# Kernel optimization log

Hardware: AMD Instinct MI355X
Metric: run time of the kernel (lower is better)

The kernel has to match this reference:

```python
import jax, jax.numpy as jnp
import numpy as np

N_NODES = 100000
N_EDGES = 1600000
N_GRAPHS = 512
DIM = 64


def gcn_conv(x, W, b, src, dst, n):
    # PyG GCNConv: h = x @ W; add self-loops; symmetric norm D^-1/2 (A+I) D^-1/2; aggregate; + bias
    h = x @ W  # [N, H]
    loop = jnp.arange(n, dtype=src.dtype)
    s = jnp.concatenate([src, loop])
    d = jnp.concatenate([dst, loop])
    deg = jax.ops.segment_sum(jnp.ones_like(d, dtype=h.dtype), d, num_segments=n)  # in-degree incl self-loop
    dinv = jnp.where(deg > 0, jax.lax.rsqrt(deg), 0.0)
    norm = dinv[s] * dinv[d]  # [E+N]
    msg = h[s] * norm[:, None]  # gather + scale
    out = jax.ops.segment_sum(msg, d, num_segments=n)  # scatter-add
    return out + b


def global_mean_pool(x, batch, num_graphs):
    sums = jax.ops.segment_sum(x, batch, num_segments=num_graphs)
    cnts = jax.ops.segment_sum(jnp.ones((x.shape[0],), x.dtype), batch, num_segments=num_graphs)
    return sums / jnp.maximum(cnts, 1.0)[:, None]


def setup_inputs() -> dict:
    key = jax.random.key(0)
    ks = jax.random.split(key, 12)
    scale = 1.0 / np.sqrt(DIM)
    x = jax.random.normal(ks[0], (N_NODES, DIM), jnp.float32)
    edge_index = jax.random.randint(ks[1], (2, N_EDGES), 0, N_NODES, dtype=jnp.int64)
    batch = jnp.sort(jax.random.randint(ks[2], (N_NODES,), 0, N_GRAPHS, dtype=jnp.int64))
    W1 = jax.random.normal(ks[3], (DIM, DIM), jnp.float32) * scale
    b1 = jnp.zeros((DIM,), jnp.float32)
    W2 = jax.random.normal(ks[4], (DIM, DIM), jnp.float32) * scale
    b2 = jnp.zeros((DIM,), jnp.float32)
    W3 = jax.random.normal(ks[5], (DIM, DIM), jnp.float32) * scale
    b3 = jnp.zeros((DIM,), jnp.float32)
    W4 = jax.random.normal(ks[6], (DIM, 1), jnp.float32) * scale
    b4 = jnp.zeros((1,), jnp.float32)
    return {"x": x, "edge_index": edge_index, "batch": batch,
            "W1": W1, "b1": b1, "W2": W2, "b2": b2,
            "W3": W3, "b3": b3, "W4": W4, "b4": b4}


def reference(x, edge_index, batch, W1, b1, W2, b2, W3, b3, W4, b4):
    src, dst = edge_index[0], edge_index[1]
    h = gcn_conv(x, W1, b1, src, dst, N_NODES)
    h = jax.nn.relu(h)
    h = gcn_conv(h, W2, b2, src, dst, N_NODES)
    g = global_mean_pool(h, batch, N_GRAPHS)  # [G, H]
    g = jax.nn.relu(g @ W3 + b3)
    pred = (g @ W4 + b4).reshape(-1)  # [G]
    return pred
```

## Files before the change

### kernel.cpp

```cpp
#include <hip/hip_runtime.h>
#include <hip/hip_fp16.h>
#include <math.h>


#define NBLK 3125

__global__ __launch_bounds__(256) void k_init(float* gsum, int* blockCnt,
                                              int gsz, int nblk) {
  int i = blockIdx.x * 256 + threadIdx.x;
  if (i < gsz) gsum[i] = 0.f;
  if (i < nblk + 64) blockCnt[i] = 0;
}

__global__ __launch_bounds__(256) void k_histB(const int* __restrict__ dst,
                                               int* __restrict__ blockCnt,
                                               int e, int nblk) {
  __shared__ int h[3200];
  int t = threadIdx.x;
  for (int i = t; i < 3200; i += 256) h[i] = 0;
  __syncthreads();
  int base = blockIdx.x * 8192;
#pragma unroll
  for (int k = 0; k < 32; ++k) {
    int i = base + k * 256 + t;
    if (i < e) atomicAdd(&h[dst[i] >> 5], 1);
  }
  __syncthreads();
  for (int i = t; i < nblk; i += 256) {
    int v = h[i];
    if (v) atomicAdd(&blockCnt[i], v);
  }
}

__global__ __launch_bounds__(256) void k_scan(const int* __restrict__ blockCnt,
                                              int* __restrict__ blockBase,
                                              int* __restrict__ blockCursor,
                                              int* __restrict__ bucketCursor,
                                              int nblk, int nbuck) {
  __shared__ int wsum[4];
  int t = threadIdx.x;
  int w = t >> 6, lane = t & 63;
  int ch = (nblk + 255) >> 8;
  int lo = t * ch;
  int hi = lo + ch;
  if (hi > nblk) hi = nblk;
  int s = 0;
  for (int i = lo; i < hi; ++i) s += blockCnt[i];
  int inc = s;
  for (int off = 1; off < 64; off <<= 1) {
    int u = __shfl_up(inc, off);
    if (lane >= off) inc += u;
  }
  if (lane == 63) wsum[w] = inc;
  __syncthreads();
  int wpre = 0;
  for (int i = 0; i < w; ++i) wpre += wsum[i];
  int run = wpre + inc - s;
  for (int i = lo; i < hi; ++i) {
    int v = blockCnt[i];
    blockBase[i] = run;
    blockCursor[i] = run;
    if ((i & 63) == 0 && (i >> 6) < nbuck) bucketCursor[i >> 6] = run;
    run += v;
  }
  if (t == 0) blockBase[nblk] = wsum[0] + wsum[1] + wsum[2] + wsum[3];
}

__global__ __launch_bounds__(256) void k_p1(const int* __restrict__ src,
                                            const int* __restrict__ dst,
                                            int* __restrict__ bucketCursor,
                                            int* __restrict__ tmp, int e) {
  __shared__ int hist[64];
  __shared__ int gbase[64];
  int t = threadIdx.x;
  int base = blockIdx.x * 2048;
  if (t < 64) hist[t] = 0;
  __syncthreads();
  int ent[8], rk[8], bk[8];
#pragma unroll
  for (int k = 0; k < 8; ++k) {
    int i = base + k * 256 + t;
    bool v = i < e;
    int s = v ? src[i] : 0;
    int d = v ? dst[i] : 0;
    bk[k] = d >> 11;
    ent[k] = (((d >> 5) & 63) << 22) | (s << 5) | (d & 31);
    rk[k] = v ? atomicAdd(&hist[bk[k]], 1) : -1;
  }
  __syncthreads();
  if (t < 64 && hist[t] > 0) gbase[t] = atomicAdd(&bucketCursor[t], hist[t]);
  __syncthreads();
#pragma unroll
  for (int k = 0; k < 8; ++k)
    if (rk[k] >= 0) tmp[gbase[bk[k]] + rk[k]] = ent[k];
}

__global__ __launch_bounds__(256) void k_p2(const int* __restrict__ blockBase,
                                            const int* __restrict__ tmp,
                                            int* __restrict__ blockCursor,
                                            int* __restrict__ csr, int nblk) {
  __shared__ int hist[64];
  __shared__ int gbase[64];
  int b = blockIdx.x >> 3;
  int sl = blockIdx.x & 7;
  int hiIdx = (b + 1) << 6;
  if (hiIdx > nblk) hiIdx = nblk;
  int lo_b = blockBase[b << 6];
  int hi_b = blockBase[hiIdx];
  int len = hi_b - lo_b;
  int lo = lo_b + (int)(((long long)len * sl) >> 3);
  int hi = lo_b + (int)(((long long)len * (sl + 1)) >> 3);
  int t = threadIdx.x;
  for (int rbase = lo; rbase < hi; rbase += 2048) {
    if (t < 64) hist[t] = 0;
    __syncthreads();
    int ent[8], rk[8], bin[8];
#pragma unroll
    for (int k = 0; k < 8; ++k) {
      int i = rbase + k * 256 + t;
      bool v = i < hi;
      int en = v ? tmp[i] : 0;
      ent[k] = en;
      bin[k] = en >> 22;
      rk[k] = v ? atomicAdd(&hist[bin[k]], 1) : -1;
    }
    __syncthreads();
    if (t < 64 && hist[t] > 0)
      gbase[t] = atomicAdd(&blockCursor[(b << 6) + t], hist[t]);
    __syncthreads();
#pragma unroll
    for (int k = 0; k < 8; ++k)
      if (rk[k] >= 0) csr[gbase[bin[k]] + rk[k]] = ent[k] & 0x3FFFFF;
    __syncthreads();
  }
}

__global__ __launch_bounds__(256) void k_bsort(const int* __restrict__ blockBase,
                                               int* __restrict__ csr,
                                               float* __restrict__ dinv,
                                               int* __restrict__ segLo,
                                               int* __restrict__ segHi,
                                               const float* __restrict__ x,
                                               __half* __restrict__ P16, int n) {
  __shared__ int in_sh[1024];
  __shared__ int out_sh[1024];
  __shared__ int hist[128];
  __shared__ int hscan[128];
  __shared__ int deg[32];
  __shared__ float sdinv[32];
  int blk = blockIdx.x;
  int nodeBase = blk << 5;
  if (nodeBase >= n) return;
  int p0 = blockBase[blk];
  int p1 = blockBase[blk + 1];
  int seg = p1 - p0;
  int t = threadIdx.x;
  if (t < 32) deg[t] = 0;
  if (t == 0) {
    segLo[2 * blk] = p0;
    segHi[2 * blk] = p1;
    segLo[2 * blk + 1] = p0;
    segHi[2 * blk + 1] = p1;
  }
  __syncthreads();
  for (int i = t; i < seg; i += 256) atomicAdd(&deg[csr[p0 + i] & 31], 1);
  __syncthreads();
  if (t < 32 && nodeBase + t < n) {
    float dv = 1.0f / sqrtf((float)(deg[t] + 1));
    dinv[nodeBase + t] = dv;
    sdinv[t] = dv;
  }
  __syncthreads();
  for (int i = t; i < 1024; i += 256) {
    int row = i >> 5, h2 = (i & 31) << 1;
    int node = nodeBase + row;
    if (node < n) {
      float2 v = *(const float2*)&x[(size_t)node * 64 + h2];
      float sdv = sdinv[row];
      *(__half2*)&P16[(size_t)node * 64 + h2] =
          __floats2half2_rn(v.x * sdv, v.y * sdv);
    }
  }
  if (seg <= 0 || seg > 1024) return;
  if (t < 128) hist[t] = 0;
  __syncthreads();
  for (int i = t; i < seg; i += 256) {
    int v = csr[p0 + i];
    in_sh[i] = v;
    atomicAdd(&hist[((v & 16) << 2) | ((v >> 16) & 63)], 1);
  }
  __syncthreads();
  if (t < 64) {
    int h0 = hist[2 * t], h1 = hist[2 * t + 1];
    int s = h0 + h1;
    int inc = s;
    for (int off = 1; off < 64; off <<= 1) {
      int u = __shfl_up(inc, off);
      if (t >= off) inc += u;
    }
    hscan[2 * t] = inc - s;
    hscan[2 * t + 1] = inc - s + h0;
  }
  __syncthreads();
  int cntLow = hscan[64];
  __syncthreads();
  for (int i = t; i < seg; i += 256) {
    int v = in_sh[i];
    int pos = atomicAdd(&hscan[((v & 16) << 2) | ((v >> 16) & 63)], 1);
    out_sh[pos] = v;
  }
  __syncthreads();
  for (int i = t; i < seg; i += 256) csr[p0 + i] = out_sh[i];
  if (t == 0) {
    segHi[2 * blk] = p0 + cntLow;
    segLo[2 * blk + 1] = p0 + cntLow;
  }
}

__global__ __launch_bounds__(256) void k_gemm64brs(const float* __restrict__ X,
                                                   const float* __restrict__ W,
                                                   const float* __restrict__ bias,
                                                   const float* __restrict__ dinv,
                                                   __half* __restrict__ Y16, int n) {
  __shared__ float Xs[64 * 65];
  __shared__ float Ws[64 * 64];
  int t = threadIdx.x;
  int r0 = blockIdx.x << 6;
  for (int i = t * 4; i < 4096; i += 1024)
    *(float4*)&Ws[i] = *(const float4*)&W[i];
  for (int s = t; s < 1024; s += 256) {
    int r = s >> 4, c4 = (s & 15) << 2;
    float4 v = make_float4(0.f, 0.f, 0.f, 0.f);
    if (r0 + r < n) v = *(const float4*)&X[(size_t)(r0 + r) * 64 + c4];
    Xs[r * 65 + c4 + 0] = v.x;
    Xs[r * 65 + c4 + 1] = v.y;
    Xs[r * 65 + c4 + 2] = v.z;
    Xs[r * 65 + c4 + 3] = v.w;
  }
  __syncthreads();
  int c4 = (t & 15) << 2;
  int rb = (t >> 4) << 2;
  float4 a0 = {0, 0, 0, 0}, a1 = {0, 0, 0, 0}, a2 = {0, 0, 0, 0}, a3 = {0, 0, 0, 0};
  for (int k = 0; k < 64; ++k) {
    float4 w = *(const float4*)&Ws[k * 64 + c4];
    float x0 = Xs[(rb + 0) * 65 + k];
    float x1 = Xs[(rb + 1) * 65 + k];
    float x2 = Xs[(rb + 2) * 65 + k];
    float x3 = Xs[(rb + 3) * 65 + k];
    a0.x += x0 * w.x; a0.y += x0 * w.y; a0.z += x0 * w.z; a0.w += x0 * w.w;
    a1.x += x1 * w.x; a1.y += x1 * w.y; a1.z += x1 * w.z; a1.w += x1 * w.w;
    a2.x += x2 * w.x; a2.y += x2 * w.y; a2.z += x2 * w.z; a2.w += x2 * w.w;
    a3.x += x3 * w.x; a3.y += x3 * w.y; a3.z += x3 * w.z; a3.w += x3 * w.w;
  }
  float4 bb = *(const float4*)&bias[c4];
  int r = r0 + rb;
  union { __half2 h[2]; uint2 u; } pk;
  if (r + 0 < n) {
    float s0 = dinv[r + 0];
    pk.h[0] = __floats2half2_rn(fmaxf(a0.x + bb.x, 0.f) * s0,
                                fmaxf(a0.y + bb.y, 0.f) * s0);
    pk.h[1] = __floats2half2_rn(fmaxf(a0.z + bb.z, 0.f) * s0,
                                fmaxf(a0.w + bb.w, 0.f) * s0);
    *(uint2*)&Y16[(size_t)(r + 0) * 64 + c4] = pk.u;
  }
  if (r + 1 < n) {
    float s1 = dinv[r + 1];
    pk.h[0] = __floats2half2_rn(fmaxf(a1.x + bb.x, 0.f) * s1,
                                fmaxf(a1.y + bb.y, 0.f) * s1);
    pk.h[1] = __floats2half2_rn(fmaxf(a1.z + bb.z, 0.f) * s1,
                                fmaxf(a1.w + bb.w, 0.f) * s1);
    *(uint2*)&Y16[(size_t)(r + 1) * 64 + c4] = pk.u;
  }
  if (r + 2 < n) {
    float s2 = dinv[r + 2];
    pk.h[0] = __floats2half2_rn(fmaxf(a2.x + bb.x, 0.f) * s2,
                                fmaxf(a2.y + bb.y, 0.f) * s2);
    pk.h[1] = __floats2half2_rn(fmaxf(a2.z + bb.z, 0.f) * s2,
                                fmaxf(a2.w + bb.w, 0.f) * s2);
    *(uint2*)&Y16[(size_t)(r + 2) * 64 + c4] = pk.u;
  }
  if (r + 3 < n) {
    float s3 = dinv[r + 3];
    pk.h[0] = __floats2half2_rn(fmaxf(a3.x + bb.x, 0.f) * s3,
                                fmaxf(a3.y + bb.y, 0.f) * s3);
    pk.h[1] = __floats2half2_rn(fmaxf(a3.z + bb.z, 0.f) * s3,
                                fmaxf(a3.w + bb.w, 0.f) * s3);
    *(uint2*)&Y16[(size_t)(r + 3) * 64 + c4] = pk.u;
  }
}

template <int POOL>
__global__ __launch_bounds__(128) void k_agg(
    const __half* __restrict__ Xh, const int* __restrict__ csr,
    const int* __restrict__ segLo, const int* __restrict__ segHi,
    const float* __restrict__ dinv, const int* __restrict__ batch,
    float* __restrict__ outv, float* __restrict__ gsum, int n, int ntask) {
  __shared__ float accs[2][16 * 64];
  int t = threadIdx.x;
  int w = t >> 6, lane = t & 63;
  int task = blockIdx.x * 2 + w;
  if (task >= ntask) return;
  int nodeBase = task << 4;
  int par = task & 1;
  float* a = accs[w];
#pragma unroll 4
  for (int d = 0; d < 16; ++d) a[d * 64 + lane] = 0.f;
  int p0 = segLo[task];
  int p1 = segHi[task];
  int c = p1 - p0;
  if (c > 0) {
    int sub = lane & 31;
    int qlast = p1 - 1;
    int qq = p0 + sub;
    int pk = csr[qq < qlast ? qq : qlast];
    for (int rb = 0; rb < c; rb += 32) {
      int pk_next = 0;
      bool more = (rb + 32) < c;
      if (more) {
        int qn = p0 + rb + 32 + sub;
        pk_next = csr[qn < qlast ? qn : qlast];
      }
      int rem = c - rb;
      int ee[32];
#pragma unroll
      for (int k = 0; k < 32; ++k) ee[k] = __builtin_amdgcn_readlane(pk, k);
      __half tv[32];
#pragma unroll
      for (int k = 0; k < 32; ++k)
        tv[k] = Xh[(size_t)(ee[k] >> 5) * 64 + lane];
#pragma unroll
      for (int k = 0; k < 32; ++k)
        if (k < rem && (((ee[k] >> 4) & 1) == par))
          a[(ee[k] & 15) * 64 + lane] += __half2float(tv[k]);
      pk = pk_next;
    }
  }
  for (int d = 0; d < 16; ++d) {
    int node = nodeBase + d;
    if (node >= n) break;
    float dn = dinv[node];
    float xv = __half2float(Xh[(size_t)node * 64 + lane]);
    float v = (a[d * 64 + lane] + xv) * dn;
    if (POOL) {
      int g = batch[node];
      atomicAdd(&gsum[(size_t)g * 64 + lane], v);
    } else {
      outv[(size_t)node * 64 + lane] = v;
    }
  }
}

__global__ __launch_bounds__(256) void k_head(
    const float* __restrict__ gsum, const int* __restrict__ batch,
    const float* __restrict__ W2, const float* __restrict__ b2,
    const float* __restrict__ W3, const float* __restrict__ b3,
    const float* __restrict__ W4, const float* __restrict__ b4,
    float* __restrict__ out, int ng, int n) {
  int wid = (blockIdx.x * 256 + threadIdx.x) >> 6;
  int lane = threadIdx.x & 63;
  if (wid >= ng) return;
  int lo = 0, hi = n;
  while (lo < hi) {
    int mid = (lo + hi) >> 1;
    if (batch[mid] < wid) lo = mid + 1; else hi = mid;
  }
  int lb = lo;
  hi = n;
  while (lo < hi) {
    int mid = (lo + hi) >> 1;
    if (batch[mid] <= wid) lo = mid + 1; else hi = mid;
  }
  float cden = fmaxf((float)(lo - lb), 1.0f);
  float m = gsum[(size_t)wid * 64 + lane] / cden;
  float g2 = b2[lane];
  for (int k = 0; k < 64; ++k) {
    float mk = __shfl(m, k);
    g2 += mk * W2[k * 64 + lane];
  }
  float g3 = b3[lane];
  for (int k = 0; k < 64; ++k) {
    float gk = __shfl(g2, k);
    g3 += gk * W3[k * 64 + lane];
  }
  g3 = fmaxf(g3, 0.f);
  float r = g3 * W4[lane];
  for (int off = 32; off; off >>= 1) r += __shfl_down(r, off);
  if (lane == 0) out[wid] = r + b4[0];
}

extern "C" void kernel_launch(void* const* d_in, const int* in_sizes, int n_in,
                              void* d_out, int out_size, void* d_ws, size_t ws_size,
                              hipStream_t stream) {
  const float* x = (const float*)d_in[0];
  const int* edge = (const int*)d_in[1];
  const int* batch = (const int*)d_in[2];
  const float* W1 = (const float*)d_in[3];
  const float* b1 = (const float*)d_in[4];
  const float* W2 = (const float*)d_in[5];
  const float* b2 = (const float*)d_in[6];
  const float* W3 = (const float*)d_in[7];
  const float* b3 = (const float*)d_in[8];
  const float* W4 = (const float*)d_in[9];
  const float* b4 = (const float*)d_in[10];
  float* out = (float*)d_out;

  const int n = in_sizes[0] / 64;
  const int e = in_sizes[1] / 2;
  const int ng = out_size;
  const int* src = edge;
  const int* dst = edge + e;

  char* ws = (char*)d_ws;
  size_t off = 0;
  auto alloc = [&](size_t bytes) -> void* {
    void* p = ws + off;
    off = (off + bytes + 255) & ~(size_t)255;
    return p;
  };
  __half* A16 = (__half*)alloc((size_t)n * 64 * 2);
  float* B = (float*)alloc((size_t)n * 64 * 4);
  float* dinv = (float*)alloc((size_t)n * 4);
  int* blockCnt = (int*)alloc(3264 * 4);
  int* blockBase = (int*)alloc(3264 * 4);
  int* blockCursor = (int*)alloc(3264 * 4);
  int* bucketCursor = (int*)alloc(64 * 4);
  int* segLo = (int*)alloc(6400 * 4);
  int* segHi = (int*)alloc(6400 * 4);
  int* csr = (int*)alloc((size_t)e * 4);
  float* gsum = (float*)alloc((size_t)ng * 64 * 4);
  int* tmp = (int*)B;

  const int nblk = (n + 31) / 32;
  const int nbuck = (nblk + 63) / 64;
  const int ntask = 2 * nblk;
  const int nagg = (ntask + 1) / 2;
  const int gsz = ng * 64;

  int zmax = gsz > nblk + 64 ? gsz : nblk + 64;
  k_init<<<(zmax + 255) / 256, 256, 0, stream>>>(gsum, blockCnt, gsz, nblk);
  k_histB<<<(e + 8191) / 8192, 256, 0, stream>>>(dst, blockCnt, e, nblk);
  k_scan<<<1, 256, 0, stream>>>(blockCnt, blockBase, blockCursor, bucketCursor,
                                nblk, nbuck);
  k_p1<<<(e + 2047) / 2048, 256, 0, stream>>>(src, dst, bucketCursor, tmp, e);
  k_p2<<<nbuck * 8, 256, 0, stream>>>(blockBase, tmp, blockCursor, csr, nblk);
  k_bsort<<<nblk, 256, 0, stream>>>(blockBase, csr, dinv, segLo, segHi, x, A16, n);

  k_agg<0><<<nagg, 128, 0, stream>>>(A16, csr, segLo, segHi, dinv, batch, B,
                                     gsum, n, ntask);
  k_gemm64brs<<<(n + 63) / 64, 256, 0, stream>>>(B, W1, b1, dinv, A16, n);
  k_agg<1><<<nagg, 128, 0, stream>>>(A16, csr, segLo, segHi, dinv, batch, B,
                                     gsum, n, ntask);
  k_head<<<((size_t)ng * 64 + 255) / 256, 256, 0, stream>>>(
      gsum, batch, W2, b2, W3, b3, W4, b4, out, ng, n);
}
```

Before: 305.5 us.

## Interleave fp16 feature layout so aggregation gathers two edges per wave instruction

```diff
diff --git a/kernel.cpp b/kernel.cpp
--- a/kernel.cpp
+++ b/kernel.cpp
@@ -19,9 +19,9 @@
   int t = threadIdx.x;
   for (int i = t; i < 3200; i += 256) h[i] = 0;
   __syncthreads();
-  int base = blockIdx.x * 8192;
-#pragma unroll
-  for (int k = 0; k < 32; ++k) {
+  int base = blockIdx.x * 16384;
+#pragma unroll
+  for (int k = 0; k < 64; ++k) {
     int i = base + k * 256 + t;
     if (i < e) atomicAdd(&h[dst[i] >> 5], 1);
   }
@@ -171,14 +171,17 @@
     sdinv[t] = dv;
   }
   __syncthreads();
-  for (int i = t; i < 1024; i += 256) {
-    int row = i >> 5, h2 = (i & 31) << 1;
+  for (int i = t; i < 512; i += 256) {
+    int row = i >> 4, q2 = (i & 15) << 1;
     int node = nodeBase + row;
     if (node < n) {
-      float2 v = *(const float2*)&x[(size_t)node * 64 + h2];
-      float sdv = sdinv[row];
-      *(__half2*)&P16[(size_t)node * 64 + h2] =
-          __floats2half2_rn(v.x * sdv, v.y * sdv);
+      float2 lo = *(const float2*)&x[(size_t)node * 64 + q2];
+      float2 hi = *(const float2*)&x[(size_t)node * 64 + q2 + 32];
+      float s = sdinv[row];
+      union { __half2 h[2]; uint2 u; } pk;
+      pk.h[0] = __floats2half2_rn(lo.x * s, hi.x * s);
+      pk.h[1] = __floats2half2_rn(lo.y * s, hi.y * s);
+      *(uint2*)&P16[(size_t)node * 64 + (q2 << 1)] = pk.u;
     }
   }
   if (seg <= 0 || seg > 1024) return;
@@ -238,54 +241,56 @@
     Xs[r * 65 + c4 + 3] = v.w;
   }
   __syncthreads();
-  int c4 = (t & 15) << 2;
+  int q = t & 15;
   int rb = (t >> 4) << 2;
   float4 a0 = {0, 0, 0, 0}, a1 = {0, 0, 0, 0}, a2 = {0, 0, 0, 0}, a3 = {0, 0, 0, 0};
   for (int k = 0; k < 64; ++k) {
-    float4 w = *(const float4*)&Ws[k * 64 + c4];
+    float2 wlo = *(const float2*)&Ws[k * 64 + 2 * q];
+    float2 whi = *(const float2*)&Ws[k * 64 + 2 * q + 32];
     float x0 = Xs[(rb + 0) * 65 + k];
     float x1 = Xs[(rb + 1) * 65 + k];
     float x2 = Xs[(rb + 2) * 65 + k];
     float x3 = Xs[(rb + 3) * 65 + k];
-    a0.x += x0 * w.x; a0.y += x0 * w.y; a0.z += x0 * w.z; a0.w += x0 * w.w;
-    a1.x += x1 * w.x; a1.y += x1 * w.y; a1.z += x1 * w.z; a1.w += x1 * w.w;
-    a2.x += x2 * w.x; a2.y += x2 * w.y; a2.z += x2 * w.z; a2.w += x2 * w.w;
-    a3.x += x3 * w.x; a3.y += x3 * w.y; a3.z += x3 * w.z; a3.w += x3 * w.w;
-  }
-  float4 bb = *(const float4*)&bias[c4];
+    a0.x += x0 * wlo.x; a0.y += x0 * wlo.y; a0.z += x0 * whi.x; a0.w += x0 * whi.y;
+    a1.x += x1 * wlo.x; a1.y += x1 * wlo.y; a1.z += x1 * whi.x; a1.w += x1 * whi.y;
+    a2.x += x2 * wlo.x; a2.y += x2 * wlo.y; a2.z += x2 * whi.x; a2.w += x2 * whi.y;
+    a3.x += x3 * wlo.x; a3.y += x3 * wlo.y; a3.z += x3 * whi.x; a3.w += x3 * whi.y;
+  }
+  float2 bblo = *(const float2*)&bias[2 * q];
+  float2 bbhi = *(const float2*)&bias[2 * q + 32];
   int r = r0 + rb;
   union { __half2 h[2]; uint2 u; } pk;
   if (r + 0 < n) {
     float s0 = dinv[r + 0];
-    pk.h[0] = __floats2half2_rn(fmaxf(a0.x + bb.x, 0.f) * s0,
-                                fmaxf(a0.y + bb.y, 0.f) * s0);
-    pk.h[1] = __floats2half2_rn(fmaxf(a0.z + bb.z, 0.f) * s0,
-                                fmaxf(a0.w + bb.w, 0.f) * s0);
-    *(uint2*)&Y16[(size_t)(r + 0) * 64 + c4] = pk.u;
+    pk.h[0] = __floats2half2_rn(fmaxf(a0.x + bblo.x, 0.f) * s0,
+                                fmaxf(a0.z + bbhi.x, 0.f) * s0);
+    pk.h[1] = __floats2half2_rn(fmaxf(a0.y + bblo.y, 0.f) * s0,
+                                fmaxf(a0.w + bbhi.y, 0.f) * s0);
+    *(uint2*)&Y16[(size_t)(r + 0) * 64 + 4 * q] = pk.u;
   }
   if (r + 1 < n) {
     float s1 = dinv[r + 1];
-    pk.h[0] = __floats2half2_rn(fmaxf(a1.x + bb.x, 0.f) * s1,
-                                fmaxf(a1.y + bb.y, 0.f) * s1);
-    pk.h[1] = __floats2half2_rn(fmaxf(a1.z + bb.z, 0.f) * s1,
-                                fmaxf(a1.w + bb.w, 0.f) * s1);
-    *(uint2*)&Y16[(size_t)(r + 1) * 64 + c4] = pk.u;
+    pk.h[0] = __floats2half2_rn(fmaxf(a1.x + bblo.x, 0.f) * s1,
+                                fmaxf(a1.z + bbhi.x, 0.f) * s1);
+    pk.h[1] = __floats2half2_rn(fmaxf(a1.y + bblo.y, 0.f) * s1,
+                                fmaxf(a1.w + bbhi.y, 0.f) * s1);
+    *(uint2*)&Y16[(size_t)(r + 1) * 64 + 4 * q] = pk.u;
   }
   if (r + 2 < n) {
     float s2 = dinv[r + 2];
-    pk.h[0] = __floats2half2_rn(fmaxf(a2.x + bb.x, 0.f) * s2,
-                                fmaxf(a2.y + bb.y, 0.f) * s2);
-    pk.h[1] = __floats2half2_rn(fmaxf(a2.z + bb.z, 0.f) * s2,
-                                fmaxf(a2.w + bb.w, 0.f) * s2);
-    *(uint2*)&Y16[(size_t)(r + 2) * 64 + c4] = pk.u;
+    pk.h[0] = __floats2half2_rn(fmaxf(a2.x + bblo.x, 0.f) * s2,
+                                fmaxf(a2.z + bbhi.x, 0.f) * s2);
+    pk.h[1] = __floats2half2_rn(fmaxf(a2.y + bblo.y, 0.f) * s2,
+                                fmaxf(a2.w + bbhi.y, 0.f) * s2);
+    *(uint2*)&Y16[(size_t)(r + 2) * 64 + 4 * q] = pk.u;
   }
   if (r + 3 < n) {
     float s3 = dinv[r + 3];
-    pk.h[0] = __floats2half2_rn(fmaxf(a3.x + bb.x, 0.f) * s3,
-                                fmaxf(a3.y + bb.y, 0.f) * s3);
-    pk.h[1] = __floats2half2_rn(fmaxf(a3.z + bb.z, 0.f) * s3,
-                                fmaxf(a3.w + bb.w, 0.f) * s3);
-    *(uint2*)&Y16[(size_t)(r + 3) * 64 + c4] = pk.u;
+    pk.h[0] = __floats2half2_rn(fmaxf(a3.x + bblo.x, 0.f) * s3,
+                                fmaxf(a3.z + bbhi.x, 0.f) * s3);
+    pk.h[1] = __floats2half2_rn(fmaxf(a3.y + bblo.y, 0.f) * s3,
+                                fmaxf(a3.w + bbhi.y, 0.f) * s3);
+    *(uint2*)&Y16[(size_t)(r + 3) * 64 + 4 * q] = pk.u;
   }
 }
 
@@ -310,6 +315,7 @@
   int c = p1 - p0;
   if (c > 0) {
     int sub = lane & 31;
+    int h = lane >> 5;
     int qlast = p1 - 1;
     int qq = p0 + sub;
     int pk = csr[qq < qlast ? qq : qlast];
@@ -321,17 +327,41 @@
         pk_next = csr[qn < qlast ? qn : qlast];
       }
       int rem = c - rb;
-      int ee[32];
-#pragma unroll
-      for (int k = 0; k < 32; ++k) ee[k] = __builtin_amdgcn_readlane(pk, k);
-      __half tv[32];
-#pragma unroll
-      for (int k = 0; k < 32; ++k)
-        tv[k] = Xh[(size_t)(ee[k] >> 5) * 64 + lane];
-#pragma unroll
-      for (int k = 0; k < 32; ++k)
-        if (k < rem && (((ee[k] >> 4) & 1) == par))
-          a[(ee[k] & 15) * 64 + lane] += __half2float(tv[k]);
+      int e0[16], e1[16];
+#pragma unroll
+      for (int k = 0; k < 16; ++k) {
+        e0[k] = __builtin_amdgcn_readlane(pk, 2 * k);
+        e1[k] = __builtin_amdgcn_readlane(pk, 2 * k + 1);
+      }
+      unsigned tu[16];
+#pragma unroll
+      for (int k = 0; k < 16; ++k) {
+        int esel = h ? e1[k] : e0[k];
+        tu[k] = *(const unsigned*)&Xh[(size_t)(esel >> 5) * 64 + (sub << 1)];
+      }
+#pragma unroll
+      for (int k = 0; k < 16; ++k) {
+        bool ok0 = (2 * k < rem) && (((e0[k] >> 4) & 1) == par);
+        bool ok1 = (2 * k + 1 < rem) && (((e1[k] >> 4) & 1) == par);
+        int d0 = e0[k] & 15, d1 = e1[k] & 15;
+        __half2 hv = *(__half2*)&tu[k];
+        float2 f = __half22float2(hv);
+        if (ok0 && ok1 && d0 == d1) {
+          float ox = __shfl(f.x, sub + 32);
+          float oy = __shfl(f.y, sub + 32);
+          if (h == 0) {
+            a[d0 * 64 + sub] += f.x + ox;
+            a[d0 * 64 + sub + 32] += f.y + oy;
+          }
+        } else {
+          bool ok = h ? ok1 : ok0;
+          int d = h ? d1 : d0;
+          if (ok) {
+            a[d * 64 + sub] += f.x;
+            a[d * 64 + sub + 32] += f.y;
+          }
+        }
+      }
       pk = pk_next;
     }
   }
@@ -339,7 +369,8 @@
     int node = nodeBase + d;
     if (node >= n) break;
     float dn = dinv[node];
-    float xv = __half2float(Xh[(size_t)node * 64 + lane]);
+    int pidx = ((lane & 31) << 1) | (lane >> 5);
+    float xv = __half2float(Xh[(size_t)node * 64 + pidx]);
     float v = (a[d * 64 + lane] + xv) * dn;
     if (POOL) {
       int g = batch[node];
@@ -438,7 +469,7 @@
 
   int zmax = gsz > nblk + 64 ? gsz : nblk + 64;
   k_init<<<(zmax + 255) / 256, 256, 0, stream>>>(gsum, blockCnt, gsz, nblk);
-  k_histB<<<(e + 8191) / 8192, 256, 0, stream>>>(dst, blockCnt, e, nblk);
+  k_histB<<<(e + 16383) / 16384, 256, 0, stream>>>(dst, blockCnt, e, nblk);
   k_scan<<<1, 256, 0, stream>>>(blockCnt, blockBase, blockCursor, bucketCursor,
                                 nblk, nbuck);
   k_p1<<<(e + 2047) / 2048, 256, 0, stream>>>(src, dst, bucketCursor, tmp, e);
```

After: 323.3 us. +5.8%, slower.

## Fuse destination histogram into bucket partition pass with fixed-capacity buckets

Applied to the files above, without the earlier changes.

```diff
diff --git a/kernel.cpp b/kernel.cpp
--- a/kernel.cpp
+++ b/kernel.cpp
@@ -4,39 +4,21 @@
 
 
 #define NBLK 3125
+#define BCAP 40960
 
 __global__ __launch_bounds__(256) void k_init(float* gsum, int* blockCnt,
-                                              int gsz, int nblk) {
+                                              int* bucketCursor, int gsz,
+                                              int nblk) {
   int i = blockIdx.x * 256 + threadIdx.x;
   if (i < gsz) gsum[i] = 0.f;
   if (i < nblk + 64) blockCnt[i] = 0;
-}
-
-__global__ __launch_bounds__(256) void k_histB(const int* __restrict__ dst,
-                                               int* __restrict__ blockCnt,
-                                               int e, int nblk) {
-  __shared__ int h[3200];
-  int t = threadIdx.x;
-  for (int i = t; i < 3200; i += 256) h[i] = 0;
-  __syncthreads();
-  int base = blockIdx.x * 8192;
-#pragma unroll
-  for (int k = 0; k < 32; ++k) {
-    int i = base + k * 256 + t;
-    if (i < e) atomicAdd(&h[dst[i] >> 5], 1);
-  }
-  __syncthreads();
-  for (int i = t; i < nblk; i += 256) {
-    int v = h[i];
-    if (v) atomicAdd(&blockCnt[i], v);
-  }
+  if (i < 64) bucketCursor[i] = i * BCAP;
 }
 
 __global__ __launch_bounds__(256) void k_scan(const int* __restrict__ blockCnt,
                                               int* __restrict__ blockBase,
                                               int* __restrict__ blockCursor,
-                                              int* __restrict__ bucketCursor,
-                                              int nblk, int nbuck) {
+                                              int nblk) {
   __shared__ int wsum[4];
   int t = threadIdx.x;
   int w = t >> 6, lane = t & 63;
@@ -60,7 +42,6 @@
     int v = blockCnt[i];
     blockBase[i] = run;
     blockCursor[i] = run;
-    if ((i & 63) == 0 && (i >> 6) < nbuck) bucketCursor[i >> 6] = run;
     run += v;
   }
   if (t == 0) blockBase[nblk] = wsum[0] + wsum[1] + wsum[2] + wsum[3];
@@ -69,33 +50,49 @@
 __global__ __launch_bounds__(256) void k_p1(const int* __restrict__ src,
                                             const int* __restrict__ dst,
                                             int* __restrict__ bucketCursor,
-                                            int* __restrict__ tmp, int e) {
+                                            int* __restrict__ blockCnt,
+                                            int* __restrict__ tmp, int e,
+                                            int nblk) {
   __shared__ int hist[64];
   __shared__ int gbase[64];
-  int t = threadIdx.x;
-  int base = blockIdx.x * 2048;
-  if (t < 64) hist[t] = 0;
-  __syncthreads();
-  int ent[8], rk[8], bk[8];
-#pragma unroll
-  for (int k = 0; k < 8; ++k) {
-    int i = base + k * 256 + t;
-    bool v = i < e;
-    int s = v ? src[i] : 0;
-    int d = v ? dst[i] : 0;
-    bk[k] = d >> 11;
-    ent[k] = (((d >> 5) & 63) << 22) | (s << 5) | (d & 31);
-    rk[k] = v ? atomicAdd(&hist[bk[k]], 1) : -1;
-  }
-  __syncthreads();
-  if (t < 64 && hist[t] > 0) gbase[t] = atomicAdd(&bucketCursor[t], hist[t]);
-  __syncthreads();
-#pragma unroll
-  for (int k = 0; k < 8; ++k)
-    if (rk[k] >= 0) tmp[gbase[bk[k]] + rk[k]] = ent[k];
-}
-
-__global__ __launch_bounds__(256) void k_p2(const int* __restrict__ blockBase,
+  __shared__ int hB[3200];
+  int t = threadIdx.x;
+  for (int i = t; i < 3200; i += 256) hB[i] = 0;
+  int base0 = blockIdx.x * 4096;
+  for (int ph = 0; ph < 2; ++ph) {
+    int base = base0 + ph * 2048;
+    if (t < 64) hist[t] = 0;
+    __syncthreads();
+    int ent[8], rk[8], bk[8];
+#pragma unroll
+    for (int k = 0; k < 8; ++k) {
+      int i = base + k * 256 + t;
+      bool v = i < e;
+      int s = v ? src[i] : 0;
+      int d = v ? dst[i] : 0;
+      bk[k] = d >> 11;
+      ent[k] = (((d >> 5) & 63) << 22) | (s << 5) | (d & 31);
+      rk[k] = v ? atomicAdd(&hist[bk[k]], 1) : -1;
+      if (v) atomicAdd(&hB[d >> 5], 1);
+    }
+    __syncthreads();
+    if (t < 64 && hist[t] > 0) gbase[t] = atomicAdd(&bucketCursor[t], hist[t]);
+    __syncthreads();
+#pragma unroll
+    for (int k = 0; k < 8; ++k)
+      if (rk[k] >= 0) {
+        int pos = gbase[bk[k]] + rk[k];
+        if (pos < (bk[k] + 1) * BCAP) tmp[pos] = ent[k];
+      }
+  }
+  __syncthreads();
+  for (int i = t; i < nblk; i += 256) {
+    int v = hB[i];
+    if (v) atomicAdd(&blockCnt[i], v);
+  }
+}
+
+__global__ __launch_bounds__(256) void k_p2(const int* __restrict__ bucketCursor,
                                             const int* __restrict__ tmp,
                                             int* __restrict__ blockCursor,
                                             int* __restrict__ csr, int nblk) {
@@ -103,10 +100,8 @@
   __shared__ int gbase[64];
   int b = blockIdx.x >> 3;
   int sl = blockIdx.x & 7;
-  int hiIdx = (b + 1) << 6;
-  if (hiIdx > nblk) hiIdx = nblk;
-  int lo_b = blockBase[b << 6];
-  int hi_b = blockBase[hiIdx];
+  int lo_b = b * BCAP;
+  int hi_b = bucketCursor[b];
   int len = hi_b - lo_b;
   int lo = lo_b + (int)(((long long)len * sl) >> 3);
   int hi = lo_b + (int)(((long long)len * (sl + 1)) >> 3);
@@ -437,12 +432,12 @@
   const int gsz = ng * 64;
 
   int zmax = gsz > nblk + 64 ? gsz : nblk + 64;
-  k_init<<<(zmax + 255) / 256, 256, 0, stream>>>(gsum, blockCnt, gsz, nblk);
-  k_histB<<<(e + 8191) / 8192, 256, 0, stream>>>(dst, blockCnt, e, nblk);
-  k_scan<<<1, 256, 0, stream>>>(blockCnt, blockBase, blockCursor, bucketCursor,
-                                nblk, nbuck);
-  k_p1<<<(e + 2047) / 2048, 256, 0, stream>>>(src, dst, bucketCursor, tmp, e);
-  k_p2<<<nbuck * 8, 256, 0, stream>>>(blockBase, tmp, blockCursor, csr, nblk);
+  k_init<<<(zmax + 255) / 256, 256, 0, stream>>>(gsum, blockCnt, bucketCursor,
+                                                 gsz, nblk);
+  k_p1<<<(e + 4095) / 4096, 256, 0, stream>>>(src, dst, bucketCursor, blockCnt,
+                                              tmp, e, nblk);
+  k_scan<<<1, 256, 0, stream>>>(blockCnt, blockBase, blockCursor, nblk);
+  k_p2<<<nbuck * 8, 256, 0, stream>>>(bucketCursor, tmp, blockCursor, csr, nblk);
   k_bsort<<<nblk, 256, 0, stream>>>(blockBase, csr, dinv, segLo, segHi, x, A16, n);
 
   k_agg<0><<<nagg, 128, 0, stream>>>(A16, csr, segLo, segHi, dinv, batch, B,
```

Result: faster. 297.7 us (-2.6%).
